# Kernel tuning notes

Hardware: AMD Instinct MI355X
Metric: run time of the kernel (lower is better)

## Reference

```python
import jax, jax.numpy as jnp
import numpy as np

BETA = 0.25

def setup_inputs() -> dict:
    key = jax.random.key(0)
    k1, k2 = jax.random.split(key)
    z = jax.random.normal(k1, (16, 256, 32, 32), dtype=jnp.float32)
    # embedding initialized uniform(-1/ne, 1/ne) in the module; scale is immaterial for correctness
    ne = 8192
    codebook = jax.random.uniform(k2, (ne, 256), dtype=jnp.float32, minval=-1.0 / ne, maxval=1.0 / ne)
    return {"z": z, "codebook": codebook}


def reference(z, codebook):
    # z: [B, C, H, W] channel-first -> channel-last [B, H, W, C]
    z_cl = jnp.transpose(z, (0, 2, 3, 1))
    # distance (up to a constant ||z||^2 term, as in the original):
    # d = ||e||^2 - 2 <z, e>, shape [B, H, W, NE]
    d = jnp.sum(codebook ** 2, axis=1) - 2.0 * jnp.einsum('bhwd,nd->bhwn', z_cl, codebook)
    index = jnp.argmin(d, axis=-1)                      # [B, H, W]
    z_q = codebook[index]                               # [B, H, W, C] gather
    # commitment + codebook losses with straight-through
    loss = jnp.mean((jax.lax.stop_gradient(z_q) - z_cl) ** 2) \
         + BETA * jnp.mean((z_q - jax.lax.stop_gradient(z_cl)) ** 2)
    z_q_st = z_cl + jax.lax.stop_gradient(z_q - z_cl)   # straight-through estimator
    z_q_cf = jnp.transpose(z_q_st, (0, 3, 1, 2))        # back to channel-first [B, C, H, W]
    return z_q_cf, index, loss
```

## Files before the change

### kernel.cpp

```cpp
#include <hip/hip_runtime.h>
#include <float.h>

#define NPIX 16384
#define NE   8192
#define KD   256
#define HW   1024
#define BCHW 262144
#define NT   8
#define DELTA 2.5e-4f
#define KMASK 0xFFFFE000u

typedef __attribute__((ext_vector_type(8))) short short8;
typedef __attribute__((ext_vector_type(4))) short short4v;
typedef __attribute__((ext_vector_type(4))) float f32x4;
typedef __attribute__((ext_vector_type(4))) unsigned int u32x4;
typedef unsigned long long u64;
typedef unsigned int u32;

__device__ __forceinline__ u32 fkey(float f) {
    u32 u = __float_as_uint(f);
    return u ^ ((u >> 31) ? 0xFFFFFFFFu : 0x80000000u);
}
__device__ __forceinline__ short bf16rne(float f) {
    u32 u = __float_as_uint(f);
    u += 0x7FFFu + ((u >> 16) & 1u);
    return (short)(u >> 16);
}
__device__ __forceinline__ float kval(u32 pk) {
    return __uint_as_float(pk & KMASK);
}

#define GLDS(gp, lp) __builtin_amdgcn_global_load_lds( \
    (const __attribute__((address_space(1))) void*)(gp), \
    (__attribute__((address_space(3))) void*)(lp), 16, 0, 0)

__global__ void vq_prep(const float* __restrict__ cb, short* __restrict__ eh,
                        float* __restrict__ e2) {
    const int row  = (blockIdx.x * 256 + threadIdx.x) >> 6;
    const int lane = threadIdx.x & 63;
    const f32x4 v = *(const f32x4*)(cb + (size_t)row * KD + lane * 4);
    short4v h;
    h[0] = bf16rne(v[0]); h[1] = bf16rne(v[1]);
    h[2] = bf16rne(v[2]); h[3] = bf16rne(v[3]);
    *(short4v*)(eh + (size_t)row * KD + lane * 4) = h;
    float s = v[0]*v[0] + v[1]*v[1] + v[2]*v[2] + v[3]*v[3];
    #pragma unroll
    for (int m = 1; m < 64; m <<= 1) s += __shfl_xor(s, m);
    if (lane == 0) e2[row] = s;
}

__global__ void vq_zh(const float* __restrict__ z, short* __restrict__ zh) {
    __shared__ float ts[64][65];
    const int b   = blockIdx.z;
    const int k0  = blockIdx.y * 64;
    const int hw0 = blockIdx.x * 64;
    const int tid = threadIdx.x;
    const int pl  = tid & 63, kk = tid >> 6;
    #pragma unroll
    for (int i = 0; i < 16; ++i) {
        const int k = kk + 4 * i;
        ts[k][pl] = z[b * BCHW + (k0 + k) * HW + hw0 + pl];
    }
    __syncthreads();
    const int tx = tid & 15, ty = tid >> 4;
    #pragma unroll
    for (int j = 0; j < 4; ++j) {
        const int p = ty + 16 * j;
        short4v v;
        #pragma unroll
        for (int q = 0; q < 4; ++q) v[q] = bf16rne(ts[tx * 4 + q][p]);
        *(short4v*)(zh + (size_t)(b * HW + hw0 + p) * KD + k0 + tx * 4) = v;
    }
}

__global__ __launch_bounds__(256, 2) void vq_gemm(
    const short* __restrict__ zh, const short* __restrict__ eh,
    u32* __restrict__ best4)
{
    __shared__ short Bs[4][4096];

    const int tid  = threadIdx.x;
    const int lane = tid & 63;
    const int w    = tid >> 6;
    const int wm   = w >> 1, wn = w & 1;
    const int p0   = blockIdx.x * 128;
    const int nb0  = blockIdx.y * (NT * 128);

    const int sr = lane >> 2;
    const int ss = (lane & 3) ^ ((sr >> 1) & 3);
    const int q   = lane >> 4;
    const int rsw = ((lane & 15) >> 1) & 3;

    u32 b1[4][4], b2[4][4];
    #pragma unroll
    for (int m = 0; m < 4; ++m)
        #pragma unroll
        for (int r = 0; r < 4; ++r) { b1[m][r] = 0xFFFFFFFFu; b2[m][r] = 0xFFFFFFFFu; }

    short8 afr[4][8];
    #pragma unroll
    for (int m = 0; m < 4; ++m) {
        const size_t rowb = (size_t)(p0 + wm * 64 + m * 16 + (lane & 15)) * KD;
        #pragma unroll
        for (int ks = 0; ks < 8; ++ks)
            afr[m][ks] = *(const short8*)(zh + rowb + ks * 32 + q * 8);
    }
    asm volatile("s_waitcnt vmcnt(0)" ::: "memory");

    #define STAGEB(nt_, t_, buf_) do {                                         \
        const int k0_ = (t_) * 32;                                             \
        const int n0_ = nb0 + (nt_) * 128;                                     \
        _Pragma("unroll")                                                      \
        for (int i_ = 0; i_ < 2; ++i_) {                                       \
            const int rb_ = w * 32 + i_ * 16;                                  \
            GLDS(eh + (size_t)(n0_ + rb_ + sr) * KD + k0_ + ss * 8,            \
                 &Bs[buf_][rb_ * 32]);                                         \
        }                                                                      \
    } while (0)

    f32x4 acc[4][4];

    STAGEB(0, 0, 0);
    STAGEB(0, 1, 1);

    #pragma unroll 1
    for (int nt = 0; nt < NT; ++nt) {
        const bool lastnt = (nt == NT - 1);
        #pragma unroll
        for (int t = 0; t < 8; ++t) {
            if (lastnt && t == 7) asm volatile("s_waitcnt vmcnt(0)" ::: "memory");
            else                  asm volatile("s_waitcnt vmcnt(2)" ::: "memory");
            __builtin_amdgcn_sched_barrier(0);
            __builtin_amdgcn_s_barrier();

            if (t < 6)        { STAGEB(nt, t + 2, (t + 2) & 3); }
            else if (!lastnt) { STAGEB(nt + 1, t - 6, (t - 6) & 3); }

            if (t == 0) {
                #pragma unroll
                for (int m = 0; m < 4; ++m)
                    #pragma unroll
                    for (int nf = 0; nf < 4; ++nf)
                        acc[m][nf] = (f32x4){0.f, 0.f, 0.f, 0.f};
            }

            short8 bfv[4];
            #pragma unroll
            for (int nf = 0; nf < 4; ++nf) {
                const int row = wn * 64 + nf * 16 + (lane & 15);
                bfv[nf] = *(const short8*)&Bs[t & 3][row * 32 + ((q ^ rsw) * 8)];
            }
            #pragma unroll
            for (int m = 0; m < 4; ++m)
                #pragma unroll
                for (int nf = 0; nf < 4; ++nf)
                    acc[m][nf] = __builtin_amdgcn_mfma_f32_16x16x32_bf16(
                        afr[m][t], bfv[nf], acc[m][nf], 0, 0, 0);

            if (t == 7) {
                const u32 nbase = (u32)(nb0 + nt * 128 + wn * 64 + (lane & 15));
                #pragma unroll
                for (int m = 0; m < 4; ++m) {
                    #pragma unroll
                    for (int r = 0; r < 4; ++r) {
                        u32 pk0 = (__float_as_uint(0.0625f - acc[m][0][r]) & KMASK) | (nbase);
                        u32 pk1 = (__float_as_uint(0.0625f - acc[m][1][r]) & KMASK) | (nbase + 16u);
                        u32 pk2 = (__float_as_uint(0.0625f - acc[m][2][r]) & KMASK) | (nbase + 32u);
                        u32 pk3 = (__float_as_uint(0.0625f - acc[m][3][r]) & KMASK) | (nbase + 48u);
                        const u32 lo01 = min(pk0, pk1), hi01 = max(pk0, pk1);
                        const u32 lo23 = min(pk2, pk3), hi23 = max(pk2, pk3);
                        const u32 m1 = min(lo01, lo23);
                        const u32 m2 = min(max(lo01, lo23), min(hi01, hi23));
                        const u32 nb1 = min(b1[m][r], m1);
                        const u32 nb2 = min(max(b1[m][r], m1), min(b2[m][r], m2));
                        b1[m][r] = nb1; b2[m][r] = nb2;
                    }
                }
            }
        }
    }
    #undef STAGEB

    const int g = lane >> 4;
    const int hs = blockIdx.y * 2 + wn;
    #pragma unroll
    for (int m = 0; m < 4; ++m) {
        #pragma unroll
        for (int r = 0; r < 4; ++r) {
            u32 a = b1[m][r], b = b2[m][r];
            u32 o[4];
            #pragma unroll
            for (int j = 0; j < 4; ++j) {
                u32 mm = a;
                #pragma unroll
                for (int msk = 1; msk < 16; msk <<= 1)
                    mm = min(mm, (u32)__shfl_xor((int)mm, msk));
                o[j] = mm;
                if (a == mm) { a = b; b = 0xFFFFFFFFu; }
            }
            if ((lane & 15) == 0) {
                const int prow = p0 + wm * 64 + m * 16 + g * 4 + r;
                u32x4 ov; ov[0] = o[0]; ov[1] = o[1]; ov[2] = o[2]; ov[3] = o[3];
                *(u32x4*)&best4[((size_t)prow * 16 + hs) * 4] = ov;
            }
        }
    }
}

__global__ __launch_bounds__(256) void vq_exact(
    const float* __restrict__ z, const float* __restrict__ cb,
    const float* __restrict__ e2, const u32* __restrict__ best4,
    u64* __restrict__ final_)
{
    __shared__ float zb[16][260];
    __shared__ u32 work[1024];
    __shared__ u32 scans[256];
    __shared__ int nwork, nscan;

    const int tid = threadIdx.x;
    const int g0  = blockIdx.x * 16;
    const int bb  = g0 >> 10, hw0 = g0 & 1023;
    const int pix = tid >> 4;
    const int hsx = tid & 15;

    if (tid == 0) { nwork = 0; nscan = 0; }
    __syncthreads();

    const u32x4 kv = *(const u32x4*)&best4[((size_t)(g0 + pix) * 16 + hsx) * 4];
    const u32 lmin = min(min(kv[0], kv[1]), min(kv[2], kv[3]));
    u32 mn = lmin;
    #pragma unroll
    for (int m = 1; m < 16; m <<= 1) mn = min(mn, (u32)__shfl_xor((int)mn, m));
    const float thr = kval(mn) + DELTA;
    const int c4 = (kval(kv[0]) <= thr ? 1 : 0) + (kval(kv[1]) <= thr ? 1 : 0)
                 + (kval(kv[2]) <= thr ? 1 : 0) + (kval(kv[3]) <= thr ? 1 : 0);
    int cnt = c4;
    #pragma unroll
    for (int m = 1; m < 16; m <<= 1) cnt += __shfl_xor(cnt, m);
    const int susp = (c4 == 4) ? 1 : 0;
    int anysusp = susp;
    #pragma unroll
    for (int m = 1; m < 16; m <<= 1) anysusp += __shfl_xor(anysusp, m);

    if (cnt == 1 && anysusp == 0) {
        if (lmin == mn) final_[g0 + pix] = (u64)(mn & 8191u);
    } else {
        if (c4 > 0) {
            const int base = atomicAdd(&nwork, c4);
            int k = 0;
            #pragma unroll
            for (int j = 0; j < 4; ++j)
                if (kval(kv[j]) <= thr)
                    work[base + (k++)] = ((u32)pix << 13) | (kv[j] & 8191u);
        }
        if (susp) scans[atomicAdd(&nscan, 1)] = ((u32)pix << 4) | (u32)hsx;
    }
    __syncthreads();
    const int nw = nwork, ns = nscan;
    if (nw == 0 && ns == 0) return;

    #pragma unroll
    for (int i = 0; i < 16; ++i) {
        const int idx = i * 256 + tid;
        const int c = idx >> 4, px = idx & 15;
        zb[px][c] = z[(size_t)bb * BCHW + (size_t)c * HW + hw0 + px];
    }
    __syncthreads();

    for (int i = tid; i < nw; i += 256) {
        const u32 e = work[i];
        const int px = (int)(e >> 13), n = (int)(e & 8191u);
        const float* er = cb + (size_t)n * KD;
        float acc = 0.f;
        #pragma unroll 4
        for (int k = 0; k < KD; k += 4) {
            const f32x4 zv = *(const f32x4*)&zb[px][k];
            const f32x4 ev = *(const f32x4*)(er + k);
            acc += zv[0]*ev[0] + zv[1]*ev[1] + zv[2]*ev[2] + zv[3]*ev[3];
        }
        const float s = 0.5f * e2[n] - acc;
        atomicMin(&final_[g0 + px], ((u64)fkey(s) << 32) | (u32)n);
    }

    for (int si = 0; si < ns; ++si) {
        const u32 e = scans[si];
        const int px = (int)(e >> 4), hx = (int)(e & 15u);
        u64 bku = ~0ULL;
        #pragma unroll
        for (int h = 0; h < 2; ++h) {
            const int ci = tid + h * 256;
            const int n = (hx >> 1) * 1024 + (ci >> 6) * 128
                        + (hx & 1) * 64 + (ci & 63);
            const float* er = cb + (size_t)n * KD;
            float acc = 0.f;
            #pragma unroll 4
            for (int k = 0; k < KD; k += 4) {
                const f32x4 zv = *(const f32x4*)&zb[px][k];
                const f32x4 ev = *(const f32x4*)(er + k);
                acc += zv[0]*ev[0] + zv[1]*ev[1] + zv[2]*ev[2] + zv[3]*ev[3];
            }
            const float s = 0.5f * e2[n] - acc;
            const u64 pk = ((u64)fkey(s) << 32) | (u32)n;
            bku = min(bku, pk);
        }
        #pragma unroll
        for (int m = 1; m < 64; m <<= 1) {
            const u64 o = (u64)__shfl_xor((long long)bku, m);
            bku = min(bku, o);
        }
        if ((tid & 63) == 0) atomicMin(&final_[g0 + px], bku);
    }
}

__global__ __launch_bounds__(256) void vq_out_kernel(
    const float* __restrict__ z, const float* __restrict__ cb,
    const u64* __restrict__ final_, float* __restrict__ out,
    float* __restrict__ idxf, float* __restrict__ loss)
{
    __shared__ float zq[32][257];
    __shared__ int   nidx[32];

    const int tid = threadIdx.x;
    const int p0  = blockIdx.x * 32;
    const int bb  = p0 >> 10;
    const int hw0 = p0 & 1023;

    if (tid < 32) {
        const int n = (int)((u32)final_[p0 + tid] & 8191u);
        nidx[tid] = n;
        idxf[p0 + tid] = (float)n;
    }
    __syncthreads();

    {
        const int r = tid >> 3, i = tid & 7;
        const float* src = cb + (size_t)nidx[r] * KD;
        #pragma unroll
        for (int j = 0; j < 8; ++j) {
            const int col = i * 4 + j * 32;
            const f32x4 v = *(const f32x4*)(src + col);
            zq[r][col + 0] = v[0]; zq[r][col + 1] = v[1];
            zq[r][col + 2] = v[2]; zq[r][col + 3] = v[3];
        }
    }
    __syncthreads();

    const int p4 = (tid & 7) * 4;
    const int cg = tid >> 3;
    float ls = 0.f;
    #pragma unroll
    for (int ii = 0; ii < 8; ++ii) {
        const int c = cg + 32 * ii;
        const size_t e = (size_t)bb * BCHW + (size_t)c * HW + hw0 + p4;
        const f32x4 zv = *(const f32x4*)(z + e);
        f32x4 v;
        v[0] = zq[p4 + 0][c]; v[1] = zq[p4 + 1][c];
        v[2] = zq[p4 + 2][c]; v[3] = zq[p4 + 3][c];
        *(f32x4*)(out + e) = v;
        const float d0 = v[0] - zv[0], d1 = v[1] - zv[1];
        const float d2 = v[2] - zv[2], d3 = v[3] - zv[3];
        ls += d0 * d0 + d1 * d1 + d2 * d2 + d3 * d3;
    }
    #pragma unroll
    for (int m = 1; m < 64; m <<= 1) ls += __shfl_xor(ls, m);
    if ((tid & 63) == 0) atomicAdd(loss, ls * (1.25f / 4194304.f));
}

extern "C" void kernel_launch(void* const* d_in, const int* in_sizes, int n_in,
                              void* d_out, int out_size, void* d_ws, size_t ws_size,
                              hipStream_t stream) {
    const float* z  = (const float*)d_in[0];
    const float* cb = (const float*)d_in[1];
    float* out  = (float*)d_out;
    float* idxf = out + 4194304;
    float* loss = out + 4210688;
    char* ob = (char*)d_out;
    short* zh    = (short*)ob;
    short* eh    = (short*)(ob + 8388608);
    u32*   best4 = (u32*)(ob + 12582912);

    char* ws = (char*)d_ws;
    u64*   final_ = (u64*)ws;
    float* e2     = (float*)(ws + 131072);

    hipMemsetAsync(final_, 0xFF, 131072, stream);
    hipMemsetAsync(loss, 0, 4, stream);

    vq_prep<<<2048, 256, 0, stream>>>(cb, eh, e2);
    vq_zh<<<dim3(16, 4, 16), 256, 0, stream>>>(z, zh);
    vq_gemm<<<dim3(NPIX / 128, NE / (NT * 128)), 256, 0, stream>>>(zh, eh, best4);
    vq_exact<<<NPIX / 16, 256, 0, stream>>>(z, cb, e2, best4, final_);
    vq_out_kernel<<<NPIX / 32, 256, 0, stream>>>(z, cb, final_, out, idxf, loss);
}
```

Before: 192.8 us.

## Load codebook fragments directly into registers instead of staging through LDS

Drops the LDS staging of codebook tiles, which used global_load_lds with per-step barriers. Each wave now loads its B fragments straight from global memory into a double-buffered register array, prefetching two k-steps ahead, and the occupancy hint drops to one block per SIMD. This removes the barriers and LDS traffic, but tiles shared between waves are now fetched redundantly from L2, and the extra registers lower occupancy.

```diff
diff --git a/kernel.cpp b/kernel.cpp
--- a/kernel.cpp
+++ b/kernel.cpp
@@ -29,10 +29,6 @@
 __device__ __forceinline__ float kval(u32 pk) {
     return __uint_as_float(pk & KMASK);
 }
-
-#define GLDS(gp, lp) __builtin_amdgcn_global_load_lds( \
-    (const __attribute__((address_space(1))) void*)(gp), \
-    (__attribute__((address_space(3))) void*)(lp), 16, 0, 0)
 
 __global__ void vq_prep(const float* __restrict__ cb, short* __restrict__ eh,
                         float* __restrict__ e2) {
@@ -73,23 +69,18 @@
     }
 }
 
-__global__ __launch_bounds__(256, 2) void vq_gemm(
+__global__ __launch_bounds__(256, 1) void vq_gemm(
     const short* __restrict__ zh, const short* __restrict__ eh,
     u32* __restrict__ best4)
 {
-    __shared__ short Bs[4][4096];
-
     const int tid  = threadIdx.x;
     const int lane = tid & 63;
     const int w    = tid >> 6;
     const int wm   = w >> 1, wn = w & 1;
     const int p0   = blockIdx.x * 128;
     const int nb0  = blockIdx.y * (NT * 128);
-
-    const int sr = lane >> 2;
-    const int ss = (lane & 3) ^ ((sr >> 1) & 3);
-    const int q   = lane >> 4;
-    const int rsw = ((lane & 15) >> 1) & 3;
+    const int q    = lane >> 4;
+    const int lr   = lane & 15;
 
     u32 b1[4][4], b2[4][4];
     #pragma unroll
@@ -100,42 +91,36 @@
     short8 afr[4][8];
     #pragma unroll
     for (int m = 0; m < 4; ++m) {
-        const size_t rowb = (size_t)(p0 + wm * 64 + m * 16 + (lane & 15)) * KD;
+        const size_t rowb = (size_t)(p0 + wm * 64 + m * 16 + lr) * KD;
         #pragma unroll
         for (int ks = 0; ks < 8; ++ks)
             afr[m][ks] = *(const short8*)(zh + rowb + ks * 32 + q * 8);
     }
-    asm volatile("s_waitcnt vmcnt(0)" ::: "memory");
-
-    #define STAGEB(nt_, t_, buf_) do {                                         \
-        const int k0_ = (t_) * 32;                                             \
-        const int n0_ = nb0 + (nt_) * 128;                                     \
+
+    size_t brow[4];
+    #pragma unroll
+    for (int nf = 0; nf < 4; ++nf)
+        brow[nf] = (size_t)(nb0 + wn * 64 + nf * 16 + lr) * KD + q * 8;
+
+    #define LOADB(nt_, t_, buf_) do {                                          \
         _Pragma("unroll")                                                      \
-        for (int i_ = 0; i_ < 2; ++i_) {                                       \
-            const int rb_ = w * 32 + i_ * 16;                                  \
-            GLDS(eh + (size_t)(n0_ + rb_ + sr) * KD + k0_ + ss * 8,            \
-                 &Bs[buf_][rb_ * 32]);                                         \
-        }                                                                      \
+        for (int nf_ = 0; nf_ < 4; ++nf_)                                      \
+            bfv[buf_][nf_] = *(const short8*)(eh + brow[nf_] +                 \
+                                              (size_t)(nt_) * 128 * KD +       \
+                                              (t_) * 32);                      \
     } while (0)
 
+    short8 bfv[2][4];
     f32x4 acc[4][4];
 
-    STAGEB(0, 0, 0);
-    STAGEB(0, 1, 1);
+    LOADB(0, 0, 0);
+    LOADB(0, 1, 1);
 
     #pragma unroll 1
     for (int nt = 0; nt < NT; ++nt) {
         const bool lastnt = (nt == NT - 1);
         #pragma unroll
         for (int t = 0; t < 8; ++t) {
-            if (lastnt && t == 7) asm volatile("s_waitcnt vmcnt(0)" ::: "memory");
-            else                  asm volatile("s_waitcnt vmcnt(2)" ::: "memory");
-            __builtin_amdgcn_sched_barrier(0);
-            __builtin_amdgcn_s_barrier();
-
-            if (t < 6)        { STAGEB(nt, t + 2, (t + 2) & 3); }
-            else if (!lastnt) { STAGEB(nt + 1, t - 6, (t - 6) & 3); }
-
             if (t == 0) {
                 #pragma unroll
                 for (int m = 0; m < 4; ++m)
@@ -144,21 +129,18 @@
                         acc[m][nf] = (f32x4){0.f, 0.f, 0.f, 0.f};
             }
 
-            short8 bfv[4];
-            #pragma unroll
-            for (int nf = 0; nf < 4; ++nf) {
-                const int row = wn * 64 + nf * 16 + (lane & 15);
-                bfv[nf] = *(const short8*)&Bs[t & 3][row * 32 + ((q ^ rsw) * 8)];
-            }
             #pragma unroll
             for (int m = 0; m < 4; ++m)
                 #pragma unroll
                 for (int nf = 0; nf < 4; ++nf)
                     acc[m][nf] = __builtin_amdgcn_mfma_f32_16x16x32_bf16(
-                        afr[m][t], bfv[nf], acc[m][nf], 0, 0, 0);
+                        afr[m][t], bfv[t & 1][nf], acc[m][nf], 0, 0, 0);
+
+            if (t < 6)        { LOADB(nt, t + 2, t & 1); }
+            else if (!lastnt) { LOADB(nt + 1, t - 6, t & 1); }
 
             if (t == 7) {
-                const u32 nbase = (u32)(nb0 + nt * 128 + wn * 64 + (lane & 15));
+                const u32 nbase = (u32)(nb0 + nt * 128 + wn * 64 + lr);
                 #pragma unroll
                 for (int m = 0; m < 4; ++m) {
                     #pragma unroll
@@ -179,7 +161,7 @@
             }
         }
     }
-    #undef STAGEB
+    #undef LOADB
 
     const int g = lane >> 4;
     const int hs = blockIdx.y * 2 + wn;
```

After: 262.5 us. 36.1% more time.
